# Optimization experiments

Hardware: AMD Instinct MI355X
Metric: run time of the kernel (lower is better)

Reference implementation:

```python
import jax, jax.numpy as jnp
import numpy as np

B, N, D_IN, D_OUT = 32, 256, 512, 2048
RANK, K, H_CTRL = 12, 16, 192
RESIDUAL_SCALE = 1.0


def setup_inputs() -> dict:
    key = jax.random.key(0)
    ks = jax.random.split(key, 12)
    x = jax.random.normal(ks[0], (B, N, D_IN), dtype=jnp.float32)
    shared_weight = 0.02 * jax.random.normal(ks[1], (D_OUT, D_IN), dtype=jnp.float32)
    bias = jnp.zeros((D_OUT,), dtype=jnp.float32)
    # orthogonal init for U_0 [out, in] via QR of a Gaussian
    g = jax.random.normal(ks[2], (D_OUT, D_IN), dtype=jnp.float32)
    U0, _ = jnp.linalg.qr(g, mode='reduced')  # columns orthonormal, out>=in
    left_basis = 0.02 * jax.random.normal(ks[3], (K, D_OUT, RANK), dtype=jnp.float32)
    right_basis = 0.02 * jax.random.normal(ks[4], (K, D_IN, RANK), dtype=jnp.float32)
    ctrl_dim = 3 * D_IN  # cls_mean_var pooling
    W1 = (1.0 / np.sqrt(ctrl_dim)) * jax.random.normal(ks[5], (ctrl_dim, H_CTRL), dtype=jnp.float32)
    b1 = jnp.zeros((H_CTRL,), dtype=jnp.float32)
    Wc = (1.0 / np.sqrt(H_CTRL)) * jax.random.normal(ks[6], (H_CTRL, K), dtype=jnp.float32)
    bc = jnp.zeros((K,), dtype=jnp.float32)
    Wg = (1.0 / np.sqrt(H_CTRL)) * jax.random.normal(ks[7], (H_CTRL, 1), dtype=jnp.float32)
    bg = jnp.zeros((1,), dtype=jnp.float32)
    return {"x": x, "shared_weight": shared_weight, "bias": bias, "U0": U0,
            "left_basis": left_basis, "right_basis": right_basis,
            "W1": W1, "b1": b1, "Wc": Wc, "bc": bc, "Wg": Wg, "bg": bg}


def _controller(z, W1, b1, Wc, bc, Wg, bg):
    # MLP controller: coeff head (linear) + gate head (sigmoid)
    h = jax.nn.gelu(z @ W1 + b1)
    coeff = h @ Wc + bc            # [B, K]
    gate = jax.nn.sigmoid(h @ Wg + bg)  # [B, 1]
    return coeff, gate


def reference(x, shared_weight, bias, U0, left_basis, right_basis, W1, b1, Wc, bc, Wg, bg):
    # conditioning signal: cls + mean + var (unbiased=False)
    cls = x[:, 0]
    mean = x.mean(axis=1)
    var = x.var(axis=1)  # population variance, matches unbiased=False
    z = jnp.concatenate([cls, mean, var], axis=-1)  # [B, 3*D_IN]
    coeff, gate = _controller(z, W1, b1, Wc, bc, Wg, bg)

    # tangent dictionary
    raw = jnp.einsum('kmr,kdr->kmd', left_basis, right_basis)        # [K, M, D]
    ut_raw = jnp.einsum('mi,kmj->kij', U0, raw)                       # U0^T @ raw: [K, D, D]
    sym = 0.5 * (ut_raw + jnp.swapaxes(ut_raw, -2, -1))
    tangent = raw - jnp.einsum('mi,kij->kmj', U0, sym)                # [K, M, D]
    norm = jnp.sqrt(jnp.sum(tangent * tangent, axis=(1, 2), keepdims=True))
    tangent = tangent / jnp.maximum(norm, 1e-6)

    # per-sample candidate + QR retraction (Stiefel)
    delta = jnp.einsum('bk,kmd->bmd', coeff, tangent)                 # [B, M, D]
    candidate = U0[None] + RESIDUAL_SCALE * delta
    q, r = jnp.linalg.qr(candidate, mode='reduced')                   # q: [B, M, D]
    sign = jnp.sign(jnp.diagonal(r, axis1=-2, axis2=-1))              # [B, D]
    sign = jnp.where(sign == 0, jnp.ones_like(sign), sign)
    dynamic_weight = q * sign[..., None, :]
    residual_weight = dynamic_weight - U0[None]                       # [B, M, D]

    out = x @ shared_weight.T + bias                                  # [B, N, M]
    residual_out = jnp.einsum('bnd,bmd->bnm', x, residual_weight)     # [B, N, M]
    return out + gate.reshape(-1, 1, 1) * residual_out
```

## Files before the change

### kernel.cpp

```cpp
#include <hip/hip_runtime.h>
#include <math.h>

#define B_    32
#define N_    256
#define DIN   512
#define DOUT  2048
#define RANK_ 12
#define K_    16
#define HC    192
#define CD    1536
#define P1    192
#define P2    384

typedef short short8 __attribute__((ext_vector_type(8)));
typedef float f32x4 __attribute__((ext_vector_type(4)));

__device__ inline short bf16r(float f) {
  unsigned u = __float_as_uint(f);
  unsigned r = (u + 0x7FFFu + ((u >> 16) & 1u)) >> 16;
  return (short)r;
}
__device__ inline float b16f(short s) {
  unsigned u = ((unsigned)(unsigned short)s) << 16;
  return __uint_as_float(u);
}

__global__ __launch_bounds__(256) void k_pre1(const float* __restrict__ x,
                                              const float* __restrict__ leftb,
                                              const float* __restrict__ rightb,
                                              float* __restrict__ z, float* __restrict__ Lcat,
                                              float* __restrict__ E) {
  int bx = blockIdx.x, t = threadIdx.x;
  if (bx < B_) {
    const float* xb = x + (size_t)bx * N_ * DIN;
    float* zb = z + (size_t)bx * CD;
#pragma unroll
    for (int h = 0; h < 2; ++h) {
      int d = t + h * 256;
      float s = 0.f, s2 = 0.f;
      for (int n = 0; n < N_; ++n) {
        float v = xb[(size_t)n * DIN + d];
        s += v; s2 += v * v;
      }
      float mean = s * (1.0f / N_);
      float var = s2 * (1.0f / N_) - mean * mean;
      zb[d] = xb[d];
      zb[DIN + d] = mean;
      zb[2 * DIN + d] = var;
    }
  } else {
    int idx = (bx - B_) * 256 + t;
    const int totL = DOUT * P1;
    const int totR = DIN * P1;
    if (idx < totL) {
      int m = idx / P1, j = idx - m * P1;
      int k = j / RANK_, r = j - k * RANK_;
      Lcat[idx] = leftb[((size_t)k * DOUT + m) * RANK_ + r];
    } else if (idx < totL + totR) {
      int i2 = idx - totL;
      int d = i2 / P1, j = i2 - d * P1;
      int k = j / RANK_, r = j - k * RANK_;
      E[(size_t)d * P2 + j] = rightb[((size_t)k * DIN + d) * RANK_ + r];
    }
  }
}

__device__ inline void gemm_tn_body(const float* __restrict__ A, const float* __restrict__ B,
                                    float* __restrict__ C, int i0, int j0, int Kd,
                                    int lda, int ldb, int ldc,
                                    float (*As)[33], float (*Bs)[33], int t) {
  int ii = t & 31, j4 = (t >> 5) * 4;
  float acc[4] = {0.f, 0.f, 0.f, 0.f};
  for (int kb = 0; kb < Kd; kb += 32) {
    for (int idx = t; idx < 1024; idx += 256) {
      int kk = idx >> 5, c = idx & 31;
      As[kk][c] = A[(size_t)(kb + kk) * lda + i0 + c];
      Bs[kk][c] = B[(size_t)(kb + kk) * ldb + j0 + c];
    }
    __syncthreads();
#pragma unroll 8
    for (int kk = 0; kk < 32; ++kk) {
      float a = As[kk][ii];
#pragma unroll
      for (int q = 0; q < 4; ++q) acc[q] = fmaf(a, Bs[kk][j4 + q], acc[q]);
    }
    __syncthreads();
  }
#pragma unroll
  for (int q = 0; q < 4; ++q) C[(size_t)(i0 + ii) * ldc + j0 + j4 + q] = acc[q];
}

__global__ __launch_bounds__(256) void k_pre2(const float* __restrict__ z,
                                              const float* __restrict__ W1, const float* __restrict__ b1,
                                              const float* __restrict__ Wc, const float* __restrict__ bc,
                                              const float* __restrict__ Wg, const float* __restrict__ bg,
                                              const float* __restrict__ U0, const float* __restrict__ LcatF,
                                              float* __restrict__ coeff, float* __restrict__ gate,
                                              float* __restrict__ E, float* __restrict__ GLL) {
  int bx = blockIdx.x, t = threadIdx.x;
  __shared__ float As[32][33], Bs[32][33];
  __shared__ float zs[CD];
  __shared__ float hs[HC];
  if (bx < B_) {
    const float* zb = z + (size_t)bx * CD;
    for (int i = t; i < CD; i += 256) zs[i] = zb[i];
    __syncthreads();
    if (t < HC) {
      float acc = b1[t];
      for (int d = 0; d < CD; ++d) acc = fmaf(zs[d], W1[(size_t)d * HC + t], acc);
      float x3 = acc * acc * acc;
      hs[t] = 0.5f * acc * (1.0f + tanhf(0.7978845608028654f * (acc + 0.044715f * x3)));
    }
    __syncthreads();
    if (t < K_) {
      float c = bc[t];
      for (int q = 0; q < HC; ++q) c = fmaf(hs[q], Wc[q * K_ + t], c);
      coeff[bx * K_ + t] = c;
    } else if (t == K_) {
      float g = bg[0];
      for (int q = 0; q < HC; ++q) g = fmaf(hs[q], Wg[q], g);
      gate[bx] = 1.0f / (1.0f + expf(-g));
    }
  } else if (bx < 128) {
    int idx = bx - 32;
    gemm_tn_body(U0, LcatF, E + P1, (idx & 15) * 32, (idx >> 4) * 32, DOUT, DIN, P1, P2, As, Bs, t);
  } else {
    int idx = bx - 128;
    gemm_tn_body(LcatF, LcatF, GLL, (idx % 6) * 32, (idx / 6) * 32, DOUT, P1, P1, P1, As, Bs, t);
  }
}

__global__ __launch_bounds__(256) void k_pre3(const float* __restrict__ E,
                                              const float* __restrict__ Wsh, const float* __restrict__ U0,
                                              const float* __restrict__ LcatF,
                                              float* __restrict__ GE, short* __restrict__ Bcat,
                                              short* __restrict__ Eb16, short* __restrict__ Etb16) {
  int bx = blockIdx.x, t = threadIdx.x;
  __shared__ float As[32][33], Bs[32][33];
  if (bx < 144) {
    gemm_tn_body(E, E, GE, (bx % 12) * 32, (bx / 12) * 32, DIN, P2, P2, P2, As, Bs, t);
  } else if (bx < 1360) {
    int idx = (bx - 144) * 256 + t;
    int row = idx / 152, g = idx - row * 152;
    const float* src;
    if (g < 64)       src = Wsh + (size_t)row * DIN + g * 8;
    else if (g < 128) src = U0 + (size_t)row * DIN + (g - 64) * 8;
    else              src = LcatF + (size_t)row * P1 + (g - 128) * 8;
    short8 o;
#pragma unroll
    for (int e = 0; e < 8; ++e) o[e] = bf16r(src[e]);
    *(short8*)(Bcat + (size_t)row * 1216 + g * 8) = o;
  } else {
    int idx = (bx - 1360) * 256 + t;
    int d = idx / P2, q = idx - d * P2;
    short v = bf16r(E[idx]);
    Eb16[idx] = v;
    Etb16[(size_t)q * DIN + d] = v;
  }
}

__global__ __launch_bounds__(512) void k_pre4(const float* __restrict__ GLL, const float* __restrict__ GE,
                                              const float* __restrict__ coeff,
                                              float* __restrict__ norms, float* __restrict__ cp) {
  int t = threadIdx.x;
  int k = t >> 5, lane = t & 31;
  float s1 = 0.f, s2 = 0.f, s3 = 0.f;
  for (int idx = lane; idx < RANK_ * RANK_; idx += 32) {
    int r = idx / RANK_, s = idx - r * RANK_;
    int p = k * RANK_ + r, q = k * RANK_ + s;
    float gll = GLL[p * P1 + q];
    float grr = GE[p * P2 + q];
    float gpp = GE[(P1 + p) * P2 + (P1 + q)];
    float gpr = GE[(P1 + p) * P2 + q];
    float gprt = GE[(P1 + q) * P2 + p];
    s1 += gll * grr;
    s2 += gpp * grr;
    s3 += gpr * gprt;
  }
#pragma unroll
  for (int off = 16; off > 0; off >>= 1) {
    s1 += __shfl_down(s1, off, 32);
    s2 += __shfl_down(s2, off, 32);
    s3 += __shfl_down(s3, off, 32);
  }
  if (lane == 0) norms[k] = sqrtf(fmaxf(s1 - 0.5f * (s2 + s3), 0.0f));
  __syncthreads();
  cp[t] = coeff[t] / fmaxf(norms[t & 15], 1e-6f);
}

__global__ __launch_bounds__(256) void k_pre5(const float* __restrict__ GLL, const float* __restrict__ GE,
                                              const float* __restrict__ E, const float* __restrict__ cp,
                                              short* __restrict__ M0b, short* __restrict__ Ecb) {
  int bx = blockIdx.x, t = threadIdx.x;
  if (bx < 576) {
    int idx = bx * 256 + t;
    if (idx >= P2 * P2) return;
    int p = idx / P2, q = idx - p * P2;
    float v;
    if (p < P1) {
      if (q < P1) v = GLL[p * P1 + q] - 0.75f * GE[(P1 + p) * P2 + (P1 + q)];
      else        v = -0.25f * GE[(P1 + p) * P2 + (q - P1)];
    } else {
      if (q < P1) v = -0.25f * GE[(P1 + q) * P2 + (p - P1)];
      else        v = 0.25f * GE[(p - P1) * P2 + (q - P1)];
    }
    M0b[idx] = bf16r(v);
  } else {
    int idx = (bx - 576) * 256 + t;
    int b = idx / (DIN * 48);
    int rem = idx - b * DIN * 48;
    int d = rem / 48, g = rem - d * 48;
    int q0 = g * 8;
    const float* src = E + (size_t)d * P2 + q0;
    const float* cpb = cp + b * K_;
    short8 o;
#pragma unroll
    for (int e = 0; e < 8; ++e) {
      int q = q0 + e;
      int kidx = (q % P1) / RANK_;
      o[e] = bf16r(src[e] * cpb[kidx]);
    }
    *(short8*)(Ecb + ((size_t)b * DIN + d) * P2 + q0) = o;
  }
}

template<int MSZ, int NSZ, int KD>
__global__ __launch_bounds__(256) void k_mf_nt16(const short* __restrict__ A,
                                                 const short* __restrict__ B,
                                                 short* __restrict__ C) {
  int b = blockIdx.z;
  const short* Ab = A + (size_t)b * MSZ * KD;
  short* Cb = C + (size_t)b * MSZ * NSZ;
  int c0 = blockIdx.x * 64, r0 = blockIdx.y * 64;
  __shared__ short As[64][40], Bs[64][40];
  int t = threadIdx.x;
  int l = t & 63, wid = t >> 6;
  int wr = wid >> 1, wc = wid & 1;
  int fr = l & 15, fq = l >> 4;
  int row = t >> 2, cg = t & 3;
  f32x4 acc[2][2] = {};
  for (int kt = 0; kt < KD / 32; ++kt) {
    *(short8*)&As[row][cg * 8] = *(const short8*)(Ab + (size_t)(r0 + row) * KD + kt * 32 + cg * 8);
    *(short8*)&Bs[row][cg * 8] = *(const short8*)(B + (size_t)(c0 + row) * KD + kt * 32 + cg * 8);
    __syncthreads();
    short8 af[2], bf[2];
#pragma unroll
    for (int m = 0; m < 2; ++m) af[m] = *(const short8*)&As[wr * 32 + m * 16 + fr][fq * 8];
#pragma unroll
    for (int n = 0; n < 2; ++n) bf[n] = *(const short8*)&Bs[wc * 32 + n * 16 + fr][fq * 8];
#pragma unroll
    for (int m = 0; m < 2; ++m)
#pragma unroll
      for (int n = 0; n < 2; ++n)
        acc[m][n] = __builtin_amdgcn_mfma_f32_16x16x32_bf16(af[m], bf[n], acc[m][n], 0, 0, 0);
    __syncthreads();
  }
#pragma unroll
  for (int m = 0; m < 2; ++m)
#pragma unroll
    for (int n = 0; n < 2; ++n)
#pragma unroll
      for (int j = 0; j < 4; ++j)
        Cb[(size_t)(r0 + wr * 32 + m * 16 + fq * 4 + j) * NSZ + c0 + wc * 32 + n * 16 + fr] =
            bf16r(acc[m][n][j]);
}

__global__ __launch_bounds__(256) void k_mf_G(const short* __restrict__ H,
                                              const short* __restrict__ Ec,
                                              float* __restrict__ G) {
  int b = blockIdx.z;
  const short* Ab = H + (size_t)b * DIN * P2;
  const short* Bb = Ec + (size_t)b * DIN * P2;
  float* Gb = G + (size_t)b * DIN * DIN;
  int c0 = blockIdx.x * 64, r0 = blockIdx.y * 64;
  __shared__ short As[64][40], Bs[64][40];
  int t = threadIdx.x;
  int l = t & 63, wid = t >> 6;
  int wr = wid >> 1, wc = wid & 1;
  int fr = l & 15, fq = l >> 4;
  int row = t >> 2, cg = t & 3;
  f32x4 acc[2][2] = {};
  for (int kt = 0; kt < P2 / 32; ++kt) {
    *(short8*)&As[row][cg * 8] = *(const short8*)(Ab + (size_t)(r0 + row) * P2 + kt * 32 + cg * 8);
    *(short8*)&Bs[row][cg * 8] = *(const short8*)(Bb + (size_t)(c0 + row) * P2 + kt * 32 + cg * 8);
    __syncthreads();
    short8 af[2], bf[2];
#pragma unroll
    for (int m = 0; m < 2; ++m) af[m] = *(const short8*)&As[wr * 32 + m * 16 + fr][fq * 8];
#pragma unroll
    for (int n = 0; n < 2; ++n) bf[n] = *(const short8*)&Bs[wc * 32 + n * 16 + fr][fq * 8];
#pragma unroll
    for (int m = 0; m < 2; ++m)
#pragma unroll
      for (int n = 0; n < 2; ++n)
        acc[m][n] = __builtin_amdgcn_mfma_f32_16x16x32_bf16(af[m], bf[n], acc[m][n], 0, 0, 0);
    __syncthreads();
  }
#pragma unroll
  for (int m = 0; m < 2; ++m)
#pragma unroll
    for (int n = 0; n < 2; ++n)
#pragma unroll
      for (int j = 0; j < 4; ++j) {
        int gr = r0 + wr * 32 + m * 16 + fq * 4 + j;
        int gc = c0 + wc * 32 + n * 16 + fr;
        Gb[(size_t)gr * DIN + gc] = acc[m][n][j] + (gr == gc ? 1.0f : 0.0f);
      }
}

__global__ __launch_bounds__(64) void k_chol_dp2(float* __restrict__ G, float* __restrict__ Wd,
                                                 int j0) {
  int b = blockIdx.y;
  int role = blockIdx.x;
  float* Gb = G + (size_t)b * DIN * DIN;
  __shared__ float D[64][65];
  __shared__ float Wls[64][65];
  __shared__ float dinvs[64];
  int t = threadIdx.x;
#pragma unroll 8
  for (int i = 0; i < 64; ++i) D[i][t] = Gb[(size_t)(j0 + i) * DIN + j0 + t];
  __syncthreads();
  {
    float col[64];
#pragma unroll
    for (int i = 0; i < 64; ++i) col[i] = D[i][t];
#pragma unroll
    for (int j = 0; j < 64; ++j) {
      float djj = __shfl(col[j], j);
      float rjj = sqrtf(fmaxf(djj, 1e-30f));
      float rinv = 1.0f / rjj;
      if (t == j) col[j] = rjj;
      else if (t > j) col[j] *= rinv;
      float djt = col[j];
#pragma unroll
      for (int i = j + 1; i < 64; ++i) {
        float rji = __shfl(col[j], i);
        if (i <= t) col[i] = fmaf(-rji, djt, col[i]);
      }
    }
#pragma unroll
    for (int i = 0; i < 64; ++i) D[i][t] = (i <= t) ? col[i] : 0.0f;
    dinvs[t] = 1.0f / col[t];
  }
  __syncthreads();
  if (role == 0) {
#pragma unroll 4
    for (int i = 0; i < 64; ++i) Wls[i][t] = 0.0f;
    Wls[t][t] = dinvs[t];
    for (int i = 62; i >= 0; --i) {
      float s = 0.0f;
      for (int j = i + 1; j < 64; ++j) s = fmaf(D[i][j], Wls[j][t], s);
      if (t > i) Wls[i][t] = -s * dinvs[i];
    }
    float* Wp = Wd + ((size_t)b * 8 + (j0 >> 6)) * 4096;
#pragma unroll 4
    for (int i = 0; i < 64; ++i) Wp[i * 64 + t] = Wls[i][t];
  } else {
    int c = j0 + 64 + (role - 1) * 64 + t;
    float a[64];
#pragma unroll
    for (int i = 0; i < 64; ++i) a[i] = Gb[(size_t)(j0 + i) * DIN + c];
#pragma unroll
    for (int j = 0; j < 64; ++j) {
      float aj = a[j] * dinvs[j];
      a[j] = aj;
#pragma unroll
      for (int i = j + 1; i < 64; ++i) a[i] = fmaf(-D[j][i], aj, a[i]);
    }
#pragma unroll
    for (int i = 0; i < 64; ++i) Gb[(size_t)(j0 + i) * DIN + c] = a[i];
  }
}

__global__ __launch_bounds__(256) void k_chol_tr(float* __restrict__ G, int j0, int nt) {
  int b = blockIdx.y;
  int pi = blockIdx.x;
  int ti = 0, accum = 0;
  while (pi >= accum + (nt - ti)) { accum += nt - ti; ++ti; }
  int tc = ti + (pi - accum);
  float* Gb = G + (size_t)b * DIN * DIN;
  __shared__ float As[64][65], Bs[64][65];
  int t = threadIdx.x;
  int ibase = j0 + 64 + ti * 64, cbase = j0 + 64 + tc * 64;
  for (int idx = t; idx < 4096; idx += 256) {
    int j = idx >> 6, c = idx & 63;
    As[j][c] = Gb[(size_t)(j0 + j) * DIN + ibase + c];
    Bs[j][c] = Gb[(size_t)(j0 + j) * DIN + cbase + c];
  }
  __syncthreads();
  int tx = t & 15, ty = t >> 4;
  float acc[4][4] = {};
#pragma unroll 8
  for (int k = 0; k < 64; ++k) {
    float a[4], bv[4];
#pragma unroll
    for (int u = 0; u < 4; ++u) a[u] = As[k][ty * 4 + u];
#pragma unroll
    for (int v = 0; v < 4; ++v) bv[v] = Bs[k][tx * 4 + v];
#pragma unroll
    for (int u = 0; u < 4; ++u)
#pragma unroll
      for (int v = 0; v < 4; ++v) acc[u][v] = fmaf(a[u], bv[v], acc[u][v]);
  }
#pragma unroll
  for (int u = 0; u < 4; ++u) {
    size_t ro = (size_t)(ibase + ty * 4 + u) * DIN + cbase + tx * 4;
#pragma unroll
    for (int v = 0; v < 4; ++v) Gb[ro + v] -= acc[u][v];
  }
}

__global__ __launch_bounds__(256) void k_trif(const float* __restrict__ x, const float* __restrict__ G,
                                              const float* __restrict__ Wd, short* __restrict__ ybf,
                                              short* __restrict__ ycb) {
  int b = blockIdx.y;
  int n0 = blockIdx.x * 16;
  const float* R = G + (size_t)b * DIN * DIN;
  const float* xb = x + ((size_t)b * N_ + n0) * DIN;
  __shared__ float Yl[16][517];
  __shared__ float Rs[64][65];
  __shared__ float Wds[64][65];
  __shared__ float Ytmp[16][69];
  int t = threadIdx.x;
  for (int idx = t; idx < 16 * DIN; idx += 256)
    Yl[idx >> 9][idx & 511] = xb[(size_t)(idx >> 9) * DIN + (idx & 511)];
  __syncthreads();
  int r = t & 15, cg = t >> 4;
  for (int p = 7; p >= 0; --p) {
    int j0 = p * 64;
    int kN = DIN - j0 - 64;
    float acc[4] = {0.f, 0.f, 0.f, 0.f};
    for (int kb = 0; kb < kN; kb += 64) {
      for (int idx = t; idx < 4096; idx += 256) {
        int kk = idx & 63, c = idx >> 6;
        Rs[kk][c] = R[(size_t)(j0 + c) * DIN + j0 + 64 + kb + kk];
      }
      __syncthreads();
#pragma unroll 8
      for (int kk = 0; kk < 64; ++kk) {
        float a = Yl[r][j0 + 64 + kb + kk];
#pragma unroll
        for (int v = 0; v < 4; ++v) acc[v] = fmaf(a, Rs[kk][cg * 4 + v], acc[v]);
      }
      __syncthreads();
    }
#pragma unroll
    for (int v = 0; v < 4; ++v) Ytmp[r][cg * 4 + v] = Yl[r][j0 + cg * 4 + v] - acc[v];
    const float* Wp = Wd + ((size_t)b * 8 + p) * 4096;
    for (int idx = t; idx < 4096; idx += 256) Wds[idx >> 6][idx & 63] = Wp[idx];
    __syncthreads();
    float o[4] = {0.f, 0.f, 0.f, 0.f};
#pragma unroll 8
    for (int jj = 0; jj < 64; ++jj) {
      float a = Ytmp[r][jj];
#pragma unroll
      for (int v = 0; v < 4; ++v) o[v] = fmaf(a, Wds[cg * 4 + v][jj], o[v]);
    }
    __syncthreads();
#pragma unroll
    for (int v = 0; v < 4; ++v) Yl[r][j0 + cg * 4 + v] = o[v];
    __syncthreads();
  }
  for (int idx = t; idx < 16 * DIN; idx += 256) {
    int rr = idx >> 9, c = idx & 511;
    float yv = Yl[rr][c];
    float xv = xb[(size_t)rr * DIN + c];
    size_t gi = ((size_t)b * N_ + n0 + rr) * DIN + c;
    ybf[gi] = bf16r(yv);
    ycb[gi] = bf16r(yv - xv);
  }
}

__global__ __launch_bounds__(256) void k_yEuv(const short* __restrict__ A,
                                              const short* __restrict__ B,
                                              const float* __restrict__ cp,
                                              const float* __restrict__ gate,
                                              short* __restrict__ C, short* __restrict__ vb) {
  int b = blockIdx.z;
  const short* Ab = A + (size_t)b * N_ * DIN;
  short* Cb = C + (size_t)b * N_ * P2;
  int c0 = blockIdx.x * 64, r0 = blockIdx.y * 64;
  __shared__ short As[64][40], Bs[64][40];
  __shared__ float cps[K_];
  int t = threadIdx.x;
  if (t < K_) cps[t] = cp[b * K_ + t];
  int l = t & 63, wid = t >> 6;
  int wr = wid >> 1, wc = wid & 1;
  int fr = l & 15, fq = l >> 4;
  int row = t >> 2, cg = t & 3;
  f32x4 acc[2][2] = {};
  __syncthreads();
  for (int kt = 0; kt < DIN / 32; ++kt) {
    *(short8*)&As[row][cg * 8] = *(const short8*)(Ab + (size_t)(r0 + row) * DIN + kt * 32 + cg * 8);
    *(short8*)&Bs[row][cg * 8] = *(const short8*)(B + (size_t)(c0 + row) * DIN + kt * 32 + cg * 8);
    __syncthreads();
    short8 af[2], bf[2];
#pragma unroll
    for (int m = 0; m < 2; ++m) af[m] = *(const short8*)&As[wr * 32 + m * 16 + fr][fq * 8];
#pragma unroll
    for (int n = 0; n < 2; ++n) bf[n] = *(const short8*)&Bs[wc * 32 + n * 16 + fr][fq * 8];
#pragma unroll
    for (int m = 0; m < 2; ++m)
#pragma unroll
      for (int n = 0; n < 2; ++n)
        acc[m][n] = __builtin_amdgcn_mfma_f32_16x16x32_bf16(af[m], bf[n], acc[m][n], 0, 0, 0);
    __syncthreads();
  }
  float gt = gate[b];
#pragma unroll
  for (int m = 0; m < 2; ++m)
#pragma unroll
    for (int n = 0; n < 2; ++n)
#pragma unroll
      for (int j = 0; j < 4; ++j) {
        int gr = r0 + wr * 32 + m * 16 + fq * 4 + j;
        int gc = c0 + wc * 32 + n * 16 + fr;
        float v = acc[m][n][j];
        Cb[(size_t)gr * P2 + gc] = bf16r(v);
        if (gc < P1)
          vb[((size_t)b * N_ + gr) * P1 + gc] = bf16r(gt * cps[gc / RANK_] * v);
      }
}

__global__ __launch_bounds__(256) void k_mf_w(const short* __restrict__ yE16,
                                              const short* __restrict__ Eb,
                                              const short* __restrict__ ycb,
                                              const float* __restrict__ cp,
                                              const float* __restrict__ gate,
                                              short* __restrict__ wb) {
  int b = blockIdx.z;
  const short* yEb = yE16 + (size_t)b * N_ * P2;
  int c0 = blockIdx.x * 64, r0 = blockIdx.y * 64;
  __shared__ short As[64][40], Bs[64][40];
  __shared__ float cps[K_];
  int t = threadIdx.x;
  if (t < K_) cps[t] = 0.5f * cp[b * K_ + t];
  int l = t & 63, wid = t >> 6;
  int wr = wid >> 1, wc = wid & 1;
  int fr = l & 15, fq = l >> 4;
  int row = t >> 2, cg = t & 3;
  f32x4 acc[2][2] = {};
  __syncthreads();
  for (int kt = 0; kt < P2 / 32; ++kt) {
    int ksrc0 = (kt * 32 + P1) % P2;
    short8 raw = *(const short8*)(yEb + (size_t)(r0 + row) * P2 + ksrc0 + cg * 8);
    short8 oa;
#pragma unroll
    for (int e = 0; e < 8; ++e) {
      int q = kt * 32 + cg * 8 + e;
      int kidx = (q % P1) / RANK_;
      oa[e] = bf16r(b16f(raw[e]) * cps[kidx]);
    }
    *(short8*)&As[row][cg * 8] = oa;
    *(short8*)&Bs[row][cg * 8] = *(const short8*)(Eb + (size_t)(c0 + row) * P2 + kt * 32 + cg * 8);
    __syncthreads();
    short8 af[2], bf[2];
#pragma unroll
    for (int m = 0; m < 2; ++m) af[m] = *(const short8*)&As[wr * 32 + m * 16 + fr][fq * 8];
#pragma unroll
    for (int n = 0; n < 2; ++n) bf[n] = *(const short8*)&Bs[wc * 32 + n * 16 + fr][fq * 8];
#pragma unroll
    for (int m = 0; m < 2; ++m)
#pragma unroll
      for (int n = 0; n < 2; ++n)
        acc[m][n] = __builtin_amdgcn_mfma_f32_16x16x32_bf16(af[m], bf[n], acc[m][n], 0, 0, 0);
    __syncthreads();
  }
  float gt = gate[b];
#pragma unroll
  for (int m = 0; m < 2; ++m)
#pragma unroll
    for (int n = 0; n < 2; ++n)
#pragma unroll
      for (int j = 0; j < 4; ++j) {
        int gr = r0 + wr * 32 + m * 16 + fq * 4 + j;
        int gc = c0 + wc * 32 + n * 16 + fr;
        size_t gi = ((size_t)b * N_ + gr) * DIN + gc;
        wb[gi] = bf16r(gt * (b16f(ycb[gi]) - acc[m][n][j]));
      }
}

__device__ inline short8 loadA8(const float* __restrict__ x, const short* __restrict__ wb,
                                const short* __restrict__ vb, int grow, int k0) {
  if (k0 < 512) {
    const float* p = x + (size_t)grow * 512 + k0;
    float4 f0 = *(const float4*)p;
    float4 f1 = *(const float4*)(p + 4);
    short8 o;
    o[0] = bf16r(f0.x); o[1] = bf16r(f0.y); o[2] = bf16r(f0.z); o[3] = bf16r(f0.w);
    o[4] = bf16r(f1.x); o[5] = bf16r(f1.y); o[6] = bf16r(f1.z); o[7] = bf16r(f1.w);
    return o;
  } else if (k0 < 1024) {
    return *(const short8*)(wb + (size_t)grow * 512 + k0 - 512);
  } else {
    return *(const short8*)(vb + (size_t)grow * 192 + k0 - 1024);
  }
}

__global__ __launch_bounds__(256) void k_final(
    const float* __restrict__ x, const short* __restrict__ wb, const short* __restrict__ vb,
    const short* __restrict__ Bcat, const float* __restrict__ bias, float* __restrict__ out) {
  __shared__ short As[2][4096];
  __shared__ short Bs[2][4096];
  int t = threadIdx.x;
  int c0 = blockIdx.x * 128;
  int r0 = blockIdx.y * 128;
  int l = t & 63, wid = t >> 6;
  int wr = wid >> 1, wc = wid & 1;
  int fr = l & 15, fq = l >> 4;
  f32x4 acc[4][4] = {};
  short8 ra0, ra1, rb0, rb1;
  const int row0 = t >> 2, c8 = t & 3;
  const int row1 = row0 + 64;
  ra0 = loadA8(x, wb, vb, r0 + row0, c8 * 8);
  ra1 = loadA8(x, wb, vb, r0 + row1, c8 * 8);
  rb0 = *(const short8*)(Bcat + (size_t)(c0 + row0) * 1216 + c8 * 8);
  rb1 = *(const short8*)(Bcat + (size_t)(c0 + row1) * 1216 + c8 * 8);
  *(short8*)&As[0][row0 * 32 + c8 * 8] = ra0;
  *(short8*)&As[0][row1 * 32 + c8 * 8] = ra1;
  *(short8*)&Bs[0][row0 * 32 + c8 * 8] = rb0;
  *(short8*)&Bs[0][row1 * 32 + c8 * 8] = rb1;
  __syncthreads();
  for (int kt = 0; kt < 38; ++kt) {
    int cur = kt & 1;
    if (kt + 1 < 38) {
      int k0 = (kt + 1) * 32;
      ra0 = loadA8(x, wb, vb, r0 + row0, k0 + c8 * 8);
      ra1 = loadA8(x, wb, vb, r0 + row1, k0 + c8 * 8);
      rb0 = *(const short8*)(Bcat + (size_t)(c0 + row0) * 1216 + k0 + c8 * 8);
      rb1 = *(const short8*)(Bcat + (size_t)(c0 + row1) * 1216 + k0 + c8 * 8);
    }
    short8 af[4], bf[4];
#pragma unroll
    for (int m = 0; m < 4; ++m)
      af[m] = *(const short8*)&As[cur][(wr * 64 + m * 16 + fr) * 32 + fq * 8];
#pragma unroll
    for (int n = 0; n < 4; ++n)
      bf[n] = *(const short8*)&Bs[cur][(wc * 64 + n * 16 + fr) * 32 + fq * 8];
#pragma unroll
    for (int m = 0; m < 4; ++m)
#pragma unroll
      for (int n = 0; n < 4; ++n)
        acc[m][n] = __builtin_amdgcn_mfma_f32_16x16x32_bf16(af[m], bf[n], acc[m][n], 0, 0, 0);
    __syncthreads();
    if (kt + 1 < 38) {
      int nxt = cur ^ 1;
      *(short8*)&As[nxt][row0 * 32 + c8 * 8] = ra0;
      *(short8*)&As[nxt][row1 * 32 + c8 * 8] = ra1;
      *(short8*)&Bs[nxt][row0 * 32 + c8 * 8] = rb0;
      *(short8*)&Bs[nxt][row1 * 32 + c8 * 8] = rb1;
    }
    __syncthreads();
  }
#pragma unroll
  for (int n = 0; n < 4; ++n) {
    int col = c0 + wc * 64 + n * 16 + fr;
    float bv = bias[col];
#pragma unroll
    for (int m = 0; m < 4; ++m) {
      int rbase = r0 + wr * 64 + m * 16 + fq * 4;
#pragma unroll
      for (int j = 0; j < 4; ++j)
        out[(size_t)(rbase + j) * DOUT + col] = acc[m][n][j] + bv;
    }
  }
}

extern "C" void kernel_launch(void* const* d_in, const int* in_sizes, int n_in,
                              void* d_out, int out_size, void* d_ws, size_t ws_size,
                              hipStream_t stream) {
  (void)in_sizes; (void)n_in; (void)out_size; (void)ws_size;
  const float* x     = (const float*)d_in[0];
  const float* Wsh   = (const float*)d_in[1];
  const float* bias  = (const float*)d_in[2];
  const float* U0    = (const float*)d_in[3];
  const float* leftb = (const float*)d_in[4];
  const float* rightb= (const float*)d_in[5];
  const float* W1    = (const float*)d_in[6];
  const float* b1    = (const float*)d_in[7];
  const float* Wc    = (const float*)d_in[8];
  const float* bc    = (const float*)d_in[9];
  const float* Wg    = (const float*)d_in[10];
  const float* bg    = (const float*)d_in[11];
  float* out = (float*)d_out;

  float* wsf = (float*)d_ws;
  float* z     = wsf + 0;
  float* coeff = wsf + 49152;
  float* gate  = wsf + 49664;
  float* norms = wsf + 49728;
  float* cp    = wsf + 49792;
  float* LcatF = wsf + 50304;
  float* E     = wsf + 443520;
  float* GLL   = wsf + 640128;
  float* GE    = wsf + 676992;
  short* M0b16 = (short*)(wsf + 824448);
  short* Eb16  = (short*)(wsf + 898176);
  short* Etb16 = (short*)(wsf + 996480);
  short* wb    = (short*)(wsf + 1094784);
  short* Ecb   = (short*)(wsf + 3191936);
  short* ybf   = (short*)(wsf + 3191936);
  short* vb    = (short*)(wsf + 5289088);
  short* Hb16  = (short*)(wsf + 6337664);
  short* ycb   = (short*)(wsf + 6337664);
  short* Bcat  = (short*)(wsf + 9483392);
  float* G = out;
  float* Wd = out + 8388608;
  short* yE16 = (short*)(out + 8388608 + 1048576);

  k_pre1<<<32 + 1920, 256, 0, stream>>>(x, leftb, rightb, z, LcatF, E);
  k_pre2<<<164, 256, 0, stream>>>(z, W1, b1, Wc, bc, Wg, bg, U0, LcatF, coeff, gate, E, GLL);
  k_pre3<<<2128, 256, 0, stream>>>(E, Wsh, U0, LcatF, GE, Bcat, Eb16, Etb16);
  k_pre4<<<1, 512, 0, stream>>>(GLL, GE, coeff, norms, cp);
  k_pre5<<<3648, 256, 0, stream>>>(GLL, GE, E, cp, M0b16, Ecb);
  k_mf_nt16<DIN, P2, P2><<<dim3(P2 / 64, DIN / 64, B_), 256, 0, stream>>>(Ecb, M0b16, Hb16);
  k_mf_G<<<dim3(DIN / 64, DIN / 64, B_), 256, 0, stream>>>(Hb16, Ecb, G);
  for (int p = 0; p < 8; ++p) {
    int j0 = p * 64;
    int nt = 7 - p;
    k_chol_dp2<<<dim3(nt + 1, B_), 64, 0, stream>>>(G, Wd, j0);
    if (nt > 0)
      k_chol_tr<<<dim3(nt * (nt + 1) / 2, B_), 256, 0, stream>>>(G, j0, nt);
  }
  k_trif<<<dim3(N_ / 16, B_), 256, 0, stream>>>(x, G, Wd, ybf, ycb);
  k_yEuv<<<dim3(P2 / 64, N_ / 64, B_), 256, 0, stream>>>(ybf, Etb16, cp, gate, yE16, vb);
  k_mf_w<<<dim3(DIN / 64, N_ / 64, B_), 256, 0, stream>>>(yE16, Eb16, ycb, cp, gate, wb);
  k_final<<<dim3(DOUT / 128, (B_ * N_) / 128), 256, 0, stream>>>(x, wb, vb, Bcat, bias, out);
}
```

Before: 1.562 ms.

## Split preprocessing reductions across more blocks and retile triangular solve

The per-batch column statistics now use 8 blocks per sample, each producing partial sums. The controller MLP is split across 96 blocks, and its coeff/gate heads move into k_pre4. The long-K tall GEMMs (U0^T·Lcat and Lcat^T·Lcat) are split four ways over K, with a new reduction kernel combining the partials. The triangular-solve kernel now handles 32 rows per block with 8 outputs per thread. Together these aim to fix low occupancy in the prologue kernels and to reuse R/Wd tiles across more rows, at the cost of an extra launch and extra partial-buffer traffic.

```diff
diff --git a/kernel.cpp b/kernel.cpp
--- a/kernel.cpp
+++ b/kernel.cpp
@@ -28,28 +28,25 @@
 __global__ __launch_bounds__(256) void k_pre1(const float* __restrict__ x,
                                               const float* __restrict__ leftb,
                                               const float* __restrict__ rightb,
-                                              float* __restrict__ z, float* __restrict__ Lcat,
-                                              float* __restrict__ E) {
+                                              float* __restrict__ sp, float* __restrict__ s2p,
+                                              float* __restrict__ Lcat, float* __restrict__ E) {
   int bx = blockIdx.x, t = threadIdx.x;
-  if (bx < B_) {
-    const float* xb = x + (size_t)bx * N_ * DIN;
-    float* zb = z + (size_t)bx * CD;
-#pragma unroll
-    for (int h = 0; h < 2; ++h) {
-      int d = t + h * 256;
+  if (bx < 256) {
+    int b = bx >> 3, c = bx & 7;
+    const float* xb = x + (size_t)b * N_ * DIN;
+#pragma unroll
+    for (int h2 = 0; h2 < 2; ++h2) {
+      int d = t + h2 * 256;
       float s = 0.f, s2 = 0.f;
-      for (int n = 0; n < N_; ++n) {
+      for (int n = c * 32; n < c * 32 + 32; ++n) {
         float v = xb[(size_t)n * DIN + d];
         s += v; s2 += v * v;
       }
-      float mean = s * (1.0f / N_);
-      float var = s2 * (1.0f / N_) - mean * mean;
-      zb[d] = xb[d];
-      zb[DIN + d] = mean;
-      zb[2 * DIN + d] = var;
+      sp[(size_t)(b * 8 + c) * DIN + d] = s;
+      s2p[(size_t)(b * 8 + c) * DIN + d] = s2;
     }
   } else {
-    int idx = (bx - B_) * 256 + t;
+    int idx = (bx - 256) * 256 + t;
     const int totL = DOUT * P1;
     const int totR = DIN * P1;
     if (idx < totL) {
@@ -65,13 +62,13 @@
   }
 }
 
-__device__ inline void gemm_tn_body(const float* __restrict__ A, const float* __restrict__ B,
-                                    float* __restrict__ C, int i0, int j0, int Kd,
+__device__ inline void gemm_tn_part(const float* __restrict__ A, const float* __restrict__ B,
+                                    float* __restrict__ C, int i0, int j0, int kb0, int klen,
                                     int lda, int ldb, int ldc,
                                     float (*As)[33], float (*Bs)[33], int t) {
   int ii = t & 31, j4 = (t >> 5) * 4;
   float acc[4] = {0.f, 0.f, 0.f, 0.f};
-  for (int kb = 0; kb < Kd; kb += 32) {
+  for (int kb = kb0; kb < kb0 + klen; kb += 32) {
     for (int idx = t; idx < 1024; idx += 256) {
       int kk = idx >> 5, c = idx & 31;
       As[kk][c] = A[(size_t)(kb + kk) * lda + i0 + c];
@@ -90,43 +87,76 @@
   for (int q = 0; q < 4; ++q) C[(size_t)(i0 + ii) * ldc + j0 + j4 + q] = acc[q];
 }
 
-__global__ __launch_bounds__(256) void k_pre2(const float* __restrict__ z,
+__global__ __launch_bounds__(256) void k_pre2(const float* __restrict__ x,
+                                              const float* __restrict__ sp, const float* __restrict__ s2p,
                                               const float* __restrict__ W1, const float* __restrict__ b1,
-                                              const float* __restrict__ Wc, const float* __restrict__ bc,
-                                              const float* __restrict__ Wg, const float* __restrict__ bg,
                                               const float* __restrict__ U0, const float* __restrict__ LcatF,
-                                              float* __restrict__ coeff, float* __restrict__ gate,
-                                              float* __restrict__ E, float* __restrict__ GLL) {
+                                              float* __restrict__ hgel,
+                                              float* __restrict__ Ppart, float* __restrict__ GLLpart) {
   int bx = blockIdx.x, t = threadIdx.x;
   __shared__ float As[32][33], Bs[32][33];
-  __shared__ float zs[CD];
-  __shared__ float hs[HC];
-  if (bx < B_) {
-    const float* zb = z + (size_t)bx * CD;
-    for (int i = t; i < CD; i += 256) zs[i] = zb[i];
-    __syncthreads();
-    if (t < HC) {
-      float acc = b1[t];
-      for (int d = 0; d < CD; ++d) acc = fmaf(zs[d], W1[(size_t)d * HC + t], acc);
+  __shared__ float zsh[CD];
+  __shared__ float hp[4][64];
+  if (bx < 96) {
+    int b = bx / 3, jt = bx % 3;
+    int j0 = jt * 64;
+    for (int d = t; d < CD; d += 256) {
+      float v;
+      if (d < DIN) {
+        v = x[(size_t)b * N_ * DIN + d];
+      } else {
+        int dd = d & 511;
+        float s = 0.f;
+#pragma unroll
+        for (int c2 = 0; c2 < 8; ++c2) s += sp[(size_t)(b * 8 + c2) * DIN + dd];
+        float mean = s * (1.0f / N_);
+        if (d < 2 * DIN) v = mean;
+        else {
+          float s2 = 0.f;
+#pragma unroll
+          for (int c2 = 0; c2 < 8; ++c2) s2 += s2p[(size_t)(b * 8 + c2) * DIN + dd];
+          v = s2 * (1.0f / N_) - mean * mean;
+        }
+      }
+      zsh[d] = v;
+    }
+    __syncthreads();
+    int j = t & 63, kg = t >> 6;
+    float a = 0.f;
+    for (int d = kg * 384; d < kg * 384 + 384; ++d)
+      a = fmaf(zsh[d], W1[(size_t)d * HC + j0 + j], a);
+    hp[kg][j] = a;
+    __syncthreads();
+    if (kg == 0) {
+      float acc = hp[0][j] + hp[1][j] + hp[2][j] + hp[3][j] + b1[j0 + j];
       float x3 = acc * acc * acc;
-      hs[t] = 0.5f * acc * (1.0f + tanhf(0.7978845608028654f * (acc + 0.044715f * x3)));
-    }
-    __syncthreads();
-    if (t < K_) {
-      float c = bc[t];
-      for (int q = 0; q < HC; ++q) c = fmaf(hs[q], Wc[q * K_ + t], c);
-      coeff[bx * K_ + t] = c;
-    } else if (t == K_) {
-      float g = bg[0];
-      for (int q = 0; q < HC; ++q) g = fmaf(hs[q], Wg[q], g);
-      gate[bx] = 1.0f / (1.0f + expf(-g));
-    }
-  } else if (bx < 128) {
-    int idx = bx - 32;
-    gemm_tn_body(U0, LcatF, E + P1, (idx & 15) * 32, (idx >> 4) * 32, DOUT, DIN, P1, P2, As, Bs, t);
+      float hj = 0.5f * acc * (1.0f + tanhf(0.7978845608028654f * (acc + 0.044715f * x3)));
+      hgel[b * HC + j0 + j] = hj;
+    }
+  } else if (bx < 480) {
+    int pb = bx - 96;
+    int tile = pb % 96, ks = pb / 96;
+    gemm_tn_part(U0, LcatF, Ppart + (size_t)ks * 98304, (tile & 15) * 32, (tile >> 4) * 32,
+                 ks * 512, 512, DIN, P1, P1, As, Bs, t);
   } else {
-    int idx = bx - 128;
-    gemm_tn_body(LcatF, LcatF, GLL, (idx % 6) * 32, (idx / 6) * 32, DOUT, P1, P1, P1, As, Bs, t);
+    int gb = bx - 480;
+    int tile = gb % 36, ks = gb / 36;
+    gemm_tn_part(LcatF, LcatF, GLLpart + (size_t)ks * 36864, (tile % 6) * 32, (tile / 6) * 32,
+                 ks * 512, 512, P1, P1, P1, As, Bs, t);
+  }
+}
+
+__global__ __launch_bounds__(256) void k_pre2b(const float* __restrict__ Ppart,
+                                               const float* __restrict__ GLLpart,
+                                               float* __restrict__ E, float* __restrict__ GLL) {
+  int idx = blockIdx.x * 256 + threadIdx.x;
+  if (idx < 98304) {
+    float s = Ppart[idx] + Ppart[98304 + idx] + Ppart[2 * 98304 + idx] + Ppart[3 * 98304 + idx];
+    int d = idx / P1, j = idx - d * P1;
+    E[(size_t)d * P2 + P1 + j] = s;
+  } else if (idx < 98304 + 36864) {
+    int i2 = idx - 98304;
+    GLL[i2] = GLLpart[i2] + GLLpart[36864 + i2] + GLLpart[2 * 36864 + i2] + GLLpart[3 * 36864 + i2];
   }
 }
 
@@ -138,7 +168,7 @@
   int bx = blockIdx.x, t = threadIdx.x;
   __shared__ float As[32][33], Bs[32][33];
   if (bx < 144) {
-    gemm_tn_body(E, E, GE, (bx % 12) * 32, (bx / 12) * 32, DIN, P2, P2, P2, As, Bs, t);
+    gemm_tn_part(E, E, GE, (bx % 12) * 32, (bx / 12) * 32, 0, DIN, P2, P2, P2, As, Bs, t);
   } else if (bx < 1360) {
     int idx = (bx - 144) * 256 + t;
     int row = idx / 152, g = idx - row * 152;
@@ -160,8 +190,11 @@
 }
 
 __global__ __launch_bounds__(512) void k_pre4(const float* __restrict__ GLL, const float* __restrict__ GE,
-                                              const float* __restrict__ coeff,
-                                              float* __restrict__ norms, float* __restrict__ cp) {
+                                              const float* __restrict__ hgel,
+                                              const float* __restrict__ Wc, const float* __restrict__ bc,
+                                              const float* __restrict__ Wg, const float* __restrict__ bg,
+                                              float* __restrict__ gate, float* __restrict__ cp) {
+  __shared__ float nrm[16];
   int t = threadIdx.x;
   int k = t >> 5, lane = t & 31;
   float s1 = 0.f, s2 = 0.f, s3 = 0.f;
@@ -183,9 +216,19 @@
     s2 += __shfl_down(s2, off, 32);
     s3 += __shfl_down(s3, off, 32);
   }
-  if (lane == 0) norms[k] = sqrtf(fmaxf(s1 - 0.5f * (s2 + s3), 0.0f));
+  if (lane == 0) nrm[k] = sqrtf(fmaxf(s1 - 0.5f * (s2 + s3), 0.0f));
+  int bb = t >> 4, kk = t & 15;
+  float c = bc[kk];
+  const float* hb = hgel + bb * HC;
+  for (int q = 0; q < HC; ++q) c = fmaf(hb[q], Wc[q * K_ + kk], c);
+  if (t < B_) {
+    float g = bg[0];
+    const float* hb2 = hgel + t * HC;
+    for (int q = 0; q < HC; ++q) g = fmaf(hb2[q], Wg[q], g);
+    gate[t] = 1.0f / (1.0f + expf(-g));
+  }
   __syncthreads();
-  cp[t] = coeff[t] / fmaxf(norms[t & 15], 1e-6f);
+  cp[t] = c / fmaxf(nrm[kk], 1e-6f);
 }
 
 __global__ __launch_bounds__(256) void k_pre5(const float* __restrict__ GLL, const float* __restrict__ GE,
@@ -414,22 +457,22 @@
                                               const float* __restrict__ Wd, short* __restrict__ ybf,
                                               short* __restrict__ ycb) {
   int b = blockIdx.y;
-  int n0 = blockIdx.x * 16;
+  int n0 = blockIdx.x * 32;
   const float* R = G + (size_t)b * DIN * DIN;
   const float* xb = x + ((size_t)b * N_ + n0) * DIN;
-  __shared__ float Yl[16][517];
+  __shared__ float Yl[32][513];
   __shared__ float Rs[64][65];
   __shared__ float Wds[64][65];
-  __shared__ float Ytmp[16][69];
-  int t = threadIdx.x;
-  for (int idx = t; idx < 16 * DIN; idx += 256)
+  __shared__ float Ytmp[32][65];
+  int t = threadIdx.x;
+  for (int idx = t; idx < 32 * DIN; idx += 256)
     Yl[idx >> 9][idx & 511] = xb[(size_t)(idx >> 9) * DIN + (idx & 511)];
   __syncthreads();
-  int r = t & 15, cg = t >> 4;
+  int r = t & 31, cg = t >> 5;
   for (int p = 7; p >= 0; --p) {
     int j0 = p * 64;
     int kN = DIN - j0 - 64;
-    float acc[4] = {0.f, 0.f, 0.f, 0.f};
+    float acc[8] = {};
     for (int kb = 0; kb < kN; kb += 64) {
       for (int idx = t; idx < 4096; idx += 256) {
         int kk = idx & 63, c = idx >> 6;
@@ -440,28 +483,28 @@
       for (int kk = 0; kk < 64; ++kk) {
         float a = Yl[r][j0 + 64 + kb + kk];
 #pragma unroll
-        for (int v = 0; v < 4; ++v) acc[v] = fmaf(a, Rs[kk][cg * 4 + v], acc[v]);
+        for (int v = 0; v < 8; ++v) acc[v] = fmaf(a, Rs[kk][cg * 8 + v], acc[v]);
       }
       __syncthreads();
     }
 #pragma unroll
-    for (int v = 0; v < 4; ++v) Ytmp[r][cg * 4 + v] = Yl[r][j0 + cg * 4 + v] - acc[v];
+    for (int v = 0; v < 8; ++v) Ytmp[r][cg * 8 + v] = Yl[r][j0 + cg * 8 + v] - acc[v];
     const float* Wp = Wd + ((size_t)b * 8 + p) * 4096;
     for (int idx = t; idx < 4096; idx += 256) Wds[idx >> 6][idx & 63] = Wp[idx];
     __syncthreads();
-    float o[4] = {0.f, 0.f, 0.f, 0.f};
+    float o[8] = {};
 #pragma unroll 8
     for (int jj = 0; jj < 64; ++jj) {
       float a = Ytmp[r][jj];
 #pragma unroll
-      for (int v = 0; v < 4; ++v) o[v] = fmaf(a, Wds[cg * 4 + v][jj], o[v]);
-    }
-    __syncthreads();
-#pragma unroll
-    for (int v = 0; v < 4; ++v) Yl[r][j0 + cg * 4 + v] = o[v];
-    __syncthreads();
-  }
-  for (int idx = t; idx < 16 * DIN; idx += 256) {
+      for (int v = 0; v < 8; ++v) o[v] = fmaf(a, Wds[cg * 8 + v][jj], o[v]);
+    }
+    __syncthreads();
+#pragma unroll
+    for (int v = 0; v < 8; ++v) Yl[r][j0 + cg * 8 + v] = o[v];
+    __syncthreads();
+  }
+  for (int idx = t; idx < 32 * DIN; idx += 256) {
     int rr = idx >> 9, c = idx & 511;
     float yv = Yl[rr][c];
     float xv = xb[(size_t)rr * DIN + c];
@@ -685,10 +728,8 @@
   float* out = (float*)d_out;
 
   float* wsf = (float*)d_ws;
-  float* z     = wsf + 0;
-  float* coeff = wsf + 49152;
+  float* hgel  = wsf + 0;
   float* gate  = wsf + 49664;
-  float* norms = wsf + 49728;
   float* cp    = wsf + 49792;
   float* LcatF = wsf + 50304;
   float* E     = wsf + 443520;
@@ -704,14 +745,19 @@
   short* Hb16  = (short*)(wsf + 6337664);
   short* ycb   = (short*)(wsf + 6337664);
   short* Bcat  = (short*)(wsf + 9483392);
+  float* sp      = wsf + 10728576;
+  float* s2p     = wsf + 10859648;
+  float* Ppart   = wsf + 10990720;
+  float* GLLpart = wsf + 11383936;
   float* G = out;
   float* Wd = out + 8388608;
   short* yE16 = (short*)(out + 8388608 + 1048576);
 
-  k_pre1<<<32 + 1920, 256, 0, stream>>>(x, leftb, rightb, z, LcatF, E);
-  k_pre2<<<164, 256, 0, stream>>>(z, W1, b1, Wc, bc, Wg, bg, U0, LcatF, coeff, gate, E, GLL);
+  k_pre1<<<256 + 1920, 256, 0, stream>>>(x, leftb, rightb, sp, s2p, LcatF, E);
+  k_pre2<<<624, 256, 0, stream>>>(x, sp, s2p, W1, b1, U0, LcatF, hgel, Ppart, GLLpart);
+  k_pre2b<<<528, 256, 0, stream>>>(Ppart, GLLpart, E, GLL);
   k_pre3<<<2128, 256, 0, stream>>>(E, Wsh, U0, LcatF, GE, Bcat, Eb16, Etb16);
-  k_pre4<<<1, 512, 0, stream>>>(GLL, GE, coeff, norms, cp);
+  k_pre4<<<1, 512, 0, stream>>>(GLL, GE, hgel, Wc, bc, Wg, bg, gate, cp);
   k_pre5<<<3648, 256, 0, stream>>>(GLL, GE, E, cp, M0b16, Ecb);
   k_mf_nt16<DIN, P2, P2><<<dim3(P2 / 64, DIN / 64, B_), 256, 0, stream>>>(Ecb, M0b16, Hb16);
   k_mf_G<<<dim3(DIN / 64, DIN / 64, B_), 256, 0, stream>>>(Hb16, Ecb, G);
@@ -722,7 +768,7 @@
     if (nt > 0)
       k_chol_tr<<<dim3(nt * (nt + 1) / 2, B_), 256, 0, stream>>>(G, j0, nt);
   }
-  k_trif<<<dim3(N_ / 16, B_), 256, 0, stream>>>(x, G, Wd, ybf, ycb);
+  k_trif<<<dim3(N_ / 32, B_), 256, 0, stream>>>(x, G, Wd, ybf, ycb);
   k_yEuv<<<dim3(P2 / 64, N_ / 64, B_), 256, 0, stream>>>(ybf, Etb16, cp, gate, yE16, vb);
   k_mf_w<<<dim3(DIN / 64, N_ / 64, B_), 256, 0, stream>>>(yE16, Eb16, ycb, cp, gate, wb);
   k_final<<<dim3(DOUT / 128, (B_ * N_) / 128), 256, 0, stream>>>(x, wb, vb, Bcat, bias, out);
```

New measurement: 1.534 ms. No clear change (-1.8%).
